# Performance work log

Hardware: AMD Instinct MI355X
Metric: run time of the kernel (lower is better)

The kernel has to match this reference:

```python
import jax, jax.numpy as jnp
from jax import lax
import numpy as np

N = 60000   # total nodes
B = 8       # graphs in batch
GS = N // B # nodes per graph
F = 384     # input node features
E = 600000  # edges
H = 6       # hiddenSize (hardcoded in source)
C = 10      # num_classes


def setup_inputs() -> dict:
    key = jax.random.key(0)
    ks = jax.random.split(key, 8)
    x = jax.random.normal(ks[0], (N, F), jnp.float32)
    src = jax.random.randint(ks[1], (E,), 0, N, jnp.int32)
    off = jax.random.randint(ks[2], (E,), 1, GS, jnp.int32)  # 1..GS-1 -> no self loops
    dst = (src // GS) * GS + (src % GS + off) % GS           # same-graph endpoint
    batch = jnp.arange(N, dtype=jnp.int32) // GS
    W1 = jax.random.normal(ks[3], (F, H), jnp.float32) * (1.0 / np.sqrt(F))
    b1 = jnp.zeros((H,), jnp.float32)
    W2 = jax.random.normal(ks[4], (H, C), jnp.float32) * (1.0 / np.sqrt(H))
    b2 = jnp.zeros((C,), jnp.float32)
    Wp1 = jax.random.normal(ks[5], (2 * H,), jnp.float32) * (1.0 / np.sqrt(2 * H))
    bp1 = jnp.zeros((), jnp.float32)
    Wp2 = jax.random.normal(ks[6], (2 * C,), jnp.float32) * (1.0 / np.sqrt(2 * C))
    bp2 = jnp.zeros((), jnp.float32)
    return dict(x=x, src=src, dst=dst, batch=batch, W1=W1, b1=b1, W2=W2, b2=b2,
                Wp1=Wp1, bp1=bp1, Wp2=Wp2, bp2=bp2)


def gcn_conv(x, src, dst, evalid, nvalid, W, b):
    # PyG GCNConv: h = x W; add remaining self-loops (weight 1); deg over dst;
    # norm = dinv[src]*dinv[dst]; aggregate to dst; + bias.
    n = x.shape[0]
    h = x @ W
    ef = evalid.astype(h.dtype)
    is_loop = evalid & (src == dst)
    has_loop = jax.ops.segment_sum(is_loop.astype(jnp.int32), dst, num_segments=n) > 0
    add_loop = (nvalid & ~has_loop).astype(h.dtype)
    deg = jax.ops.segment_sum(ef, dst, num_segments=n) + add_loop
    dinv = jnp.where(deg > 0, lax.rsqrt(jnp.maximum(deg, 1e-12)), 0.0)
    coef = ef * dinv[src] * dinv[dst]
    out = jax.ops.segment_sum(h[src] * coef[:, None], dst, num_segments=n)
    out = out + (add_loop * dinv * dinv)[:, None] * h
    return out + b


def edge_pool(x, src, dst, evalid, nvalid, Wp, bp):
    # PyG EdgePooling: raw = lin([x_src||x_dst]); score = softmax(raw, dst) + 0.5;
    # greedy contraction of edges by descending score; new_x = (sum over cluster) * score.
    n, f = x.shape
    raw = x[src] @ Wp[:f] + x[dst] @ Wp[f:] + bp                      # [E]
    rm = jnp.where(evalid, raw, -jnp.inf)
    m = jax.ops.segment_max(rm, dst, num_segments=n)
    m = jnp.where(jnp.isfinite(m), m, 0.0)
    ex = jnp.where(evalid, jnp.exp(raw - m[dst]), 0.0)
    s = jax.ops.segment_sum(ex, dst, num_segments=n)
    score = jnp.where(evalid, ex / jnp.where(s[dst] > 0, s[dst], 1.0), 0.0) + 0.5

    order = jnp.argsort(jnp.where(evalid, -score, jnp.inf))           # descending, invalid last

    def step(rem, edg):
        s_, d_, v_ = edg
        take = v_ & rem[s_] & rem[d_]
        rem = rem.at[s_].set(rem[s_] & ~take)
        rem = rem.at[d_].set(rem[d_] & ~take)
        return rem, take

    _, chosen_sorted = lax.scan(step, nvalid, (src[order], dst[order], evalid[order]))
    chosen = jnp.zeros_like(evalid).at[order].set(chosen_sorted)

    chf = chosen.astype(x.dtype)
    nonself = src != dst
    dead = jax.ops.segment_sum((chosen & nonself).astype(jnp.int32), dst, num_segments=n) > 0
    new_valid = nvalid & ~dead

    # merged feature: (x_src + x_dst) * score at slot src; unmatched: x * 1
    added = jnp.zeros_like(x).at[src].add((chf * nonself.astype(x.dtype))[:, None] * x[dst])
    scale = 1.0 + jnp.zeros((n,), x.dtype).at[src].add(chf * (score - 1.0))
    new_x = jnp.where(new_valid[:, None], (x + added) * scale[:, None], 0.0)

    # cluster map (dst of chosen edge -> src slot), remap + coalesce (dedup) edges
    merged_src = jnp.full((n,), -1, jnp.int32).at[dst].max(jnp.where(chosen, src, -1))
    cmap = jnp.where(merged_src >= 0, merged_src, jnp.arange(n, dtype=jnp.int32))
    ns, nd = cmap[src], cmap[dst]
    ns_k = jnp.where(evalid, ns, n)  # push invalid edges to the end
    order2 = jnp.lexsort((nd, ns_k))
    ss, dd = ns_k[order2], nd[order2]
    diff = (ss[1:] != ss[:-1]) | (dd[1:] != dd[:-1])
    first = jnp.concatenate([jnp.ones((1,), bool), diff])
    new_evalid = jnp.zeros_like(evalid).at[order2].set(first & evalid[order2])
    return new_x, ns, nd, new_evalid, new_valid


def _forward(x, src, dst, batch, W1, b1, W2, b2, Wp1, bp1, Wp2, bp2):
    evalid = jnp.ones((src.shape[0],), bool)
    nvalid = jnp.ones((x.shape[0],), bool)
    h = jax.nn.relu(gcn_conv(x, src, dst, evalid, nvalid, W1, b1))
    # dropout: identity in eval mode
    h, s1, d1, ev1, nv1 = edge_pool(h, src, dst, evalid, nvalid, Wp1, bp1)
    h = gcn_conv(h, s1, d1, ev1, nv1, W2, b2)
    h, s2, d2, ev2, nv2 = edge_pool(h, s1, d1, ev1, nv1, Wp2, bp2)
    nvf = nv2.astype(h.dtype)
    cnt = jax.ops.segment_sum(nvf, batch, num_segments=B)
    sm = jax.ops.segment_sum(h * nvf[:, None], batch, num_segments=B)
    g = sm / cnt[:, None]
    return jax.nn.log_softmax(g, axis=1)


def reference(x, src, dst, batch, W1, b1, W2, b2, Wp1, bp1, Wp2, bp2):
    return _forward(x, src, dst, batch, W1, b1, W2, b2, Wp1, bp1, Wp2, bp2)
```

## Files before the change

### kernel.cpp

```cpp
#include <hip/hip_runtime.h>
#include <math.h>

#define NN 60000
#define BB 8
#define GS 7500
#define FF 384
#define EE 600000
#define HH 6
#define CC 10
#define HT_BITS 20
#define HT_SIZE (1u << HT_BITS)
#define HT_MASK (HT_SIZE - 1u)
#define TPB 256
#define CAP 80000
#define REMW ((GS + 31) / 32)
#define GPAD 32
#define SCAN_B 1024
#define NBLK ((NN + SCAN_B - 1) / SCAN_B)
static_assert(NBLK <= 64, "scan2 assumes <=64 blocks");

static inline int ngrid(int n) { return (n + TPB - 1) / TPB; }

__device__ __forceinline__ unsigned long long mkprio(float sc, int e) {
  return (((unsigned long long)__float_as_uint(sc)) << 32) |
         (unsigned int)(~(unsigned int)e);
}

__global__ void k_mm1(const float* __restrict__ x, const float* __restrict__ W,
                      float* __restrict__ out) {
  __shared__ float Ws[FF * HH];
  for (int i = threadIdx.x; i < FF * HH; i += blockDim.x) Ws[i] = W[i];
  __syncthreads();
  int wave = threadIdx.x >> 6, lane = threadIdx.x & 63;
  int node = blockIdx.x * 4 + wave;
  if (node >= NN) return;
  const float* xr = x + (size_t)node * FF;
  float acc[HH] = {0.f, 0.f, 0.f, 0.f, 0.f, 0.f};
  for (int k = lane; k < FF; k += 64) {
    float xv = xr[k];
#pragma unroll
    for (int j = 0; j < HH; j++) acc[j] += xv * Ws[k * HH + j];
  }
#pragma unroll
  for (int j = 0; j < HH; j++) {
#pragma unroll
    for (int o = 32; o > 0; o >>= 1) acc[j] += __shfl_down(acc[j], o, 64);
  }
  if (lane == 0) {
#pragma unroll
    for (int j = 0; j < HH; j++) out[(size_t)node * HH + j] = acc[j];
  }
}

__global__ void k_prep(float* __restrict__ deg, unsigned char* __restrict__ hasloop,
                       int* __restrict__ gcntsA,
                       int* __restrict__ gcntsB, float* __restrict__ gsum,
                       float* __restrict__ gcnt, const unsigned char* __restrict__ nvin,
                       unsigned char* __restrict__ nvout, float* __restrict__ scale,
                       int* __restrict__ merged, int* __restrict__ partner,
                       unsigned long long* __restrict__ bestA,
                       unsigned long long* __restrict__ bestB,
                       unsigned char* __restrict__ remG) {
  int v = blockIdx.x * blockDim.x + threadIdx.x;
  if (v >= NN) return;
  deg[v] = 0.f;
  hasloop[v] = 0;
  unsigned char nvv = nvin ? nvin[v] : 1;
  nvout[v] = nvv;
  remG[v] = nvv;
  bestA[v] = 0ULL;
  bestB[v] = 0ULL;
  scale[v] = 1.0f;
  if (merged) merged[v] = -1;
  partner[v] = -1;
  if (v < BB * GPAD) { gcntsA[v] = 0; gcntsB[v] = 0; }
  if (v < BB * CC) gsum[v] = 0.f;
  if (v < BB) gcnt[v] = 0.f;
}

__global__ void k_deg(const int* __restrict__ src, const int* __restrict__ dst,
                      const unsigned char* __restrict__ ev, float* __restrict__ deg,
                      unsigned char* __restrict__ hasloop) {
  int e = blockIdx.x * blockDim.x + threadIdx.x;
  if (e >= EE) return;
  if (ev && !ev[e]) return;
  int d = dst[e];
  atomicAdd(&deg[d], 1.0f);
  if (src[e] == d) hasloop[d] = 1;
}

__global__ __launch_bounds__(1024) void k_scan1(const float* __restrict__ deg,
                                                int* __restrict__ rowstart,
                                                int* __restrict__ bsum) {
  __shared__ int tmp[SCAN_B];
  int t = threadIdx.x;
  int i = blockIdx.x * SCAN_B + t;
  int v = (i < NN) ? (int)deg[i] : 0;
  tmp[t] = v;
  __syncthreads();
  for (int o = 1; o < SCAN_B; o <<= 1) {
    int y = (t >= o) ? tmp[t - o] : 0;
    __syncthreads();
    tmp[t] += y;
    __syncthreads();
  }
  if (i < NN) rowstart[i] = tmp[t] - v;
  if (t == SCAN_B - 1) bsum[blockIdx.x] = tmp[t];
}

__global__ void k_scan2(int* __restrict__ bsum, int* __restrict__ rowstartNN) {
  int t = threadIdx.x;
  int v = (t < NBLK) ? bsum[t] : 0;
  int x = v;
#pragma unroll
  for (int o = 1; o < 64; o <<= 1) {
    int y = __shfl_up(x, o, 64);
    if (t >= o) x += y;
  }
  if (t < NBLK) bsum[t] = x - v;
  if (t == NBLK - 1) *rowstartNN = x;
}

__global__ void k_scan3(int* __restrict__ rowstart, const int* __restrict__ bsum,
                        int* __restrict__ fill, const float* __restrict__ deg,
                        const unsigned char* __restrict__ hasloop,
                        const unsigned char* __restrict__ nv, float* __restrict__ dinv,
                        unsigned char* __restrict__ addloop) {
  int i = blockIdx.x * blockDim.x + threadIdx.x;
  if (i >= NN) return;
  int r = rowstart[i] + bsum[i >> 10];
  rowstart[i] = r;
  fill[i] = r;
  int nvv = nv ? (int)nv[i] : 1;
  unsigned char al = (nvv && !hasloop[i]) ? 1 : 0;
  float d = deg[i] + (float)al;
  dinv[i] = d > 0.f ? 1.0f / sqrtf(fmaxf(d, 1e-12f)) : 0.f;
  addloop[i] = al;
}

__global__ void k_scatter(const int* __restrict__ src, const int* __restrict__ dst,
                          const unsigned char* __restrict__ ev, int* __restrict__ fill,
                          int* __restrict__ csrS, int* __restrict__ csrE) {
  int e = blockIdx.x * blockDim.x + threadIdx.x;
  if (e >= EE) return;
  if (ev && !ev[e]) return;
  int d = dst[e];
  int p = atomicAdd(&fill[d], 1);
  csrS[p] = src[e];
  csrE[p] = e;
}

template <int FD>
__global__ void k_agg_gather(const int* __restrict__ rowstart, const int* __restrict__ csrS,
                             const float* __restrict__ dinv, const float* __restrict__ h,
                             float* __restrict__ out) {
  int v = blockIdx.x * blockDim.x + threadIdx.x;
  if (v >= NN) return;
  int b0 = rowstart[v], b1 = rowstart[v + 1];
  float acc[FD];
#pragma unroll
  for (int j = 0; j < FD; j++) acc[j] = 0.f;
  float dv = dinv[v];
  for (int i = b0; i < b1; i++) {
    int s = csrS[i];
    float c = dinv[s] * dv;
    const float* hr = h + (size_t)s * FD;
#pragma unroll
    for (int j = 0; j < FD; j++) acc[j] += hr[j] * c;
  }
#pragma unroll
  for (int j = 0; j < FD; j++) out[(size_t)v * FD + j] = acc[j];
}

__global__ void k_gcn_fin(const float* __restrict__ h, const float* __restrict__ dinv,
                          const unsigned char* __restrict__ addloop, const float* __restrict__ b,
                          float* __restrict__ out, int fd, int relu) {
  int v = blockIdx.x * blockDim.x + threadIdx.x;
  if (v >= NN) return;
  float c = addloop[v] ? dinv[v] * dinv[v] : 0.f;
  for (int j = 0; j < fd; j++) {
    float o = out[(size_t)v * fd + j] + c * h[(size_t)v * fd + j] + b[j];
    if (relu) o = fmaxf(o, 0.f);
    out[(size_t)v * fd + j] = o;
  }
}

__global__ void k_raw(const float* __restrict__ x, const int* __restrict__ src,
                      const int* __restrict__ dst, const unsigned char* __restrict__ ev,
                      const float* __restrict__ Wp, const float* __restrict__ bp,
                      float* __restrict__ raw, int fd) {
  int e = blockIdx.x * blockDim.x + threadIdx.x;
  if (e >= EE) return;
  if (ev && !ev[e]) return;
  int s = src[e], d = dst[e];
  float r = bp[0];
  for (int j = 0; j < fd; j++) r += x[(size_t)s * fd + j] * Wp[j];
  for (int j = 0; j < fd; j++) r += x[(size_t)d * fd + j] * Wp[fd + j];
  raw[e] = r;
}

__global__ void k_sm_gather(const int* __restrict__ rowstart, const int* __restrict__ csrE,
                            const float* __restrict__ raw, float* __restrict__ mval,
                            float* __restrict__ ssum) {
  int v = blockIdx.x * blockDim.x + threadIdx.x;
  if (v >= NN) return;
  int b0 = rowstart[v], b1 = rowstart[v + 1];
  float m = -INFINITY;
  for (int i = b0; i < b1; i++) m = fmaxf(m, raw[csrE[i]]);
  if (b1 == b0) m = 0.f;
  float s = 0.f;
  for (int i = b0; i < b1; i++) s += expf(raw[csrE[i]] - m);
  mval[v] = m;
  ssum[v] = s;
}

__global__ void k_r1post(const int* __restrict__ src, const int* __restrict__ dst,
                         const float* __restrict__ raw, const float* __restrict__ mval,
                         const float* __restrict__ ssum,
                         const unsigned char* __restrict__ ev, const unsigned char* __restrict__ remG,
                         float* __restrict__ score, unsigned long long* __restrict__ bestA,
                         unsigned char* __restrict__ chosen) {
  int e = blockIdx.x * blockDim.x + threadIdx.x;
  if (e >= EE) return;
  chosen[e] = 0;
  if (ev && !ev[e]) return;
  int s = src[e], d = dst[e];
  if (!remG[s] || !remG[d]) return;
  float sd = ssum[d];
  float sc = expf(raw[e] - mval[d]) / (sd > 0.f ? sd : 1.0f) + 0.5f;
  score[e] = sc;
  unsigned long long p = mkprio(sc, e);
  if (p > bestA[s]) atomicMax(&bestA[s], p);
  if (d != s && p > bestA[d]) atomicMax(&bestA[d], p);
}

__global__ void k_r1sel(const int* __restrict__ src, const int* __restrict__ dst,
                        const float* __restrict__ score, const unsigned char* __restrict__ ev,
                        unsigned char* __restrict__ remG,
                        const unsigned long long* __restrict__ bestA,
                        unsigned long long* __restrict__ bestB,
                        unsigned char* __restrict__ chosen, ulonglong2* __restrict__ recs,
                        int* __restrict__ gcnts) {
  __shared__ int wcnt[TPB / 64][BB];
  __shared__ int bbase[BB];
  int e = blockIdx.x * blockDim.x + threadIdx.x;
  int w = threadIdx.x >> 6, lane = threadIdx.x & 63;
  int keep = 0, s = 0, d = 0, g = 0;
  unsigned long long p = 0;
  if (e < EE && (!ev || ev[e])) {
    s = src[e];
    d = dst[e];
    g = s / GS;
    if (remG[s] && remG[d]) {
      p = mkprio(score[e], e);
      if (bestA[s] == p && bestA[d] == p) {
        chosen[e] = 1;
        remG[s] = 0;
        remG[d] = 0;
      } else {
        keep = 1;
        bestB[s] = 0ULL;
        bestB[d] = 0ULL;
      }
    }
  }
  int myrank = 0;
#pragma unroll
  for (int gg = 0; gg < BB; gg++) {
    unsigned long long m = __ballot(keep && g == gg);
    if (keep && g == gg) myrank = __popcll(m & ((1ULL << lane) - 1ULL));
    if (lane == 0) wcnt[w][gg] = __popcll(m);
  }
  __syncthreads();
  if (threadIdx.x < BB) {
    int gg = threadIdx.x, tot = 0;
#pragma unroll
    for (int ww = 0; ww < TPB / 64; ww++) {
      int c = wcnt[ww][gg];
      wcnt[ww][gg] = tot;
      tot += c;
    }
    bbase[gg] = tot ? atomicAdd(&gcnts[gg * GPAD], tot) : 0;
  }
  __syncthreads();
  if (keep)
    recs[(size_t)g * CAP + bbase[g] + wcnt[w][g] + myrank] =
        make_ulonglong2(p, (((unsigned long long)(unsigned int)s) << 32) | (unsigned int)d);
}

__global__ void k_gpost(const ulonglong2* __restrict__ recs, const int* __restrict__ gcnts,
                        const unsigned char* __restrict__ remG,
                        unsigned long long* __restrict__ bestC, int* __restrict__ gcntsOut) {
  int g = blockIdx.y;
  if (blockIdx.x == 0 && threadIdx.x == 0) gcntsOut[g * GPAD] = 0;
  int n = gcnts[g * GPAD];
  const ulonglong2* lst = recs + (size_t)g * CAP;
  int stride = gridDim.x * blockDim.x;
  for (int i = blockIdx.x * blockDim.x + threadIdx.x; i < n; i += stride) {
    ulonglong2 r = lst[i];
    int s = (int)(r.y >> 32), d = (int)(r.y & 0xFFFFFFFFu);
    if (remG[s] && remG[d]) {
      if (r.x > bestC[s]) atomicMax(&bestC[s], r.x);
      if (d != s && r.x > bestC[d]) atomicMax(&bestC[d], r.x);
    }
  }
}

__global__ void k_gsel(const ulonglong2* __restrict__ recsIn, const int* __restrict__ gcntsIn,
                       unsigned char* __restrict__ remG,
                       const unsigned long long* __restrict__ bestC,
                       unsigned long long* __restrict__ bestN,
                       unsigned char* __restrict__ chosen, ulonglong2* __restrict__ recsOut,
                       int* __restrict__ gcntsOut) {
  int g = blockIdx.y;
  int n = gcntsIn[g * GPAD];
  const ulonglong2* lst = recsIn + (size_t)g * CAP;
  ulonglong2* outl = recsOut + (size_t)g * CAP;
  int lane = threadIdx.x & 63;
  int stride = gridDim.x * blockDim.x;
  for (int i = blockIdx.x * blockDim.x + threadIdx.x; i - lane < n; i += stride) {
    int keep = 0;
    ulonglong2 r;
    if (i < n) {
      r = lst[i];
      int s = (int)(r.y >> 32), d = (int)(r.y & 0xFFFFFFFFu);
      if (remG[s] && remG[d]) {
        if (bestC[s] == r.x && bestC[d] == r.x) {
          int e = (int)(~(unsigned int)(r.x & 0xFFFFFFFFu));
          chosen[e] = 1;
          remG[s] = 0;
          remG[d] = 0;
        } else {
          keep = 1;
          bestN[s] = 0ULL;
          bestN[d] = 0ULL;
        }
      }
    }
    unsigned long long m = __ballot(keep);
    int tot = __popcll(m);
    int pre = __popcll(m & ((1ULL << lane) - 1ULL));
    int b0 = 0;
    if (lane == 0 && tot) b0 = atomicAdd(&gcntsOut[g * GPAD], tot);
    b0 = __shfl(b0, 0, 64);
    if (keep) outl[b0 + pre] = r;
  }
}

__global__ __launch_bounds__(1024) void k_match_g(ulonglong2* __restrict__ recs0,
                                                  ulonglong2* __restrict__ recs1,
                                                  const int* __restrict__ gcnts,
                                                  const unsigned char* __restrict__ remG,
                                                  unsigned char* __restrict__ chosen) {
  __shared__ unsigned long long best[GS];
  __shared__ unsigned int remB[REMW];
  __shared__ int cnt_next;
  const int g = blockIdx.x;
  const int base = g * GS;
  const int t = threadIdx.x, nth = blockDim.x;
  const int lane = t & 63;

  for (int w = t; w < REMW; w += nth) {
    unsigned int bits = 0;
    int v0 = w * 32;
    if (v0 + 32 <= GS) {
      const unsigned int* p4 = (const unsigned int*)(remG + base + v0);
#pragma unroll
      for (int q = 0; q < 8; q++) {
        unsigned int x4 = p4[q];
        bits |= ((x4 & 1u) << (q * 4)) | (((x4 >> 8) & 1u) << (q * 4 + 1)) |
                (((x4 >> 16) & 1u) << (q * 4 + 2)) | (((x4 >> 24) & 1u) << (q * 4 + 3));
      }
    } else {
      for (int b = 0; b < 32; b++) {
        int v = v0 + b;
        if (v < GS) bits |= (remG[base + v] ? 1u : 0u) << b;
      }
    }
    remB[w] = bits;
  }
  for (int i = t; i < GS; i += nth) best[i] = 0ULL;
  __syncthreads();

  ulonglong2* bufs[2] = {recs0 + (size_t)g * CAP, recs1 + (size_t)g * CAP};
  int n = gcnts[g * GPAD];
  int cur = 0;
  int guard = 0;

  while (n > 0) {
    if (++guard > 100000) break;
    for (int i0 = 0; i0 < n; i0 += nth * 4) {
      ulonglong2 r[4];
      int have[4];
#pragma unroll
      for (int k = 0; k < 4; k++) {
        int i = i0 + t + k * nth;
        have[k] = i < n;
        if (have[k]) r[k] = bufs[cur][i];
      }
#pragma unroll
      for (int k = 0; k < 4; k++) {
        if (!have[k]) continue;
        int ls = (int)(r[k].y >> 32) - base, ld = (int)(r[k].y & 0xFFFFFFFFu) - base;
        if (((remB[ls >> 5] >> (ls & 31)) & 1u) && ((remB[ld >> 5] >> (ld & 31)) & 1u)) {
          if (r[k].x > best[ls]) atomicMax(&best[ls], r[k].x);
          if (ld != ls && r[k].x > best[ld]) atomicMax(&best[ld], r[k].x);
        }
      }
    }
    if (t == 0) cnt_next = 0;
    __syncthreads();
    for (int i0 = 0; i0 < n; i0 += nth * 4) {
      ulonglong2 r[4];
      int have[4];
#pragma unroll
      for (int k = 0; k < 4; k++) {
        int i = i0 + t + k * nth;
        have[k] = i < n;
        if (have[k]) r[k] = bufs[cur][i];
      }
#pragma unroll
      for (int k = 0; k < 4; k++) {
        int keep = 0;
        int ls = 0, ld = 0;
        if (have[k]) {
          ls = (int)(r[k].y >> 32) - base;
          ld = (int)(r[k].y & 0xFFFFFFFFu) - base;
          if (((remB[ls >> 5] >> (ls & 31)) & 1u) && ((remB[ld >> 5] >> (ld & 31)) & 1u)) {
            if (best[ls] == r[k].x && best[ld] == r[k].x) {
              int e = (int)(~(unsigned int)(r[k].x & 0xFFFFFFFFu));
              chosen[e] = 1;
              atomicAnd(&remB[ls >> 5], ~(1u << (ls & 31)));
              atomicAnd(&remB[ld >> 5], ~(1u << (ld & 31)));
            } else {
              keep = 1;
            }
          }
        }
        unsigned long long m = __ballot(keep);
        int tot = __popcll(m);
        int pre = __popcll(m & ((1ULL << lane) - 1ULL));
        int b0 = 0;
        if (lane == 0 && tot) b0 = atomicAdd(&cnt_next, tot);
        b0 = __shfl(b0, 0, 64);
        if (keep) bufs[cur ^ 1][b0 + pre] = r[k];
      }
    }
    __syncthreads();
    n = cnt_next;
    if (n < 4096) {
      for (int i = t; i < n; i += nth) {
        ulonglong2 r = bufs[cur ^ 1][i];
        best[(int)(r.y >> 32) - base] = 0ULL;
        best[(int)(r.y & 0xFFFFFFFFu) - base] = 0ULL;
      }
    } else {
      for (int i = t; i < GS; i += nth) best[i] = 0ULL;
    }
    __syncthreads();
    cur ^= 1;
  }
}

__global__ void k_pool_edge(const int* __restrict__ src, const int* __restrict__ dst,
                            const unsigned char* __restrict__ chosen, const float* __restrict__ score,
                            unsigned char* __restrict__ nvout, float* __restrict__ scale,
                            int* __restrict__ partner, int* __restrict__ merged) {
  int e = blockIdx.x * blockDim.x + threadIdx.x;
  if (e >= EE) return;
  if (!chosen[e]) return;
  int s = src[e], d = dst[e];
  scale[s] = score[e];
  if (merged) merged[d] = s;
  if (s != d) {
    nvout[d] = 0;
    partner[s] = d;
  }
}

__global__ void k_newx_mm2(const float* __restrict__ h1, const int* __restrict__ partner,
                           const float* __restrict__ scale, const unsigned char* __restrict__ nvout,
                           const float* __restrict__ W2, float* __restrict__ h2pre) {
  int v = blockIdx.x * blockDim.x + threadIdx.x;
  if (v >= NN) return;
  float sc = scale[v];
  int ok = nvout[v];
  int p = partner[v];
  float nx[HH];
#pragma unroll
  for (int j = 0; j < HH; j++) {
    float a = h1[(size_t)v * HH + j];
    if (p >= 0) a += h1[(size_t)p * HH + j];
    nx[j] = ok ? a * sc : 0.f;
  }
#pragma unroll
  for (int c = 0; c < CC; c++) {
    float a = 0.f;
#pragma unroll
    for (int j = 0; j < HH; j++) a += nx[j] * W2[j * CC + c];
    h2pre[(size_t)v * CC + c] = a;
  }
}

__device__ __forceinline__ unsigned int ht_hash(unsigned long long key) {
  return (unsigned int)((key * 0x9E3779B97F4A7C15ULL) >> 44) & HT_MASK;
}

__global__ void k_remap_ins(const int* __restrict__ src, const int* __restrict__ dst,
                            const int* __restrict__ merged, int* __restrict__ ns,
                            int* __restrict__ nd, unsigned long long* __restrict__ htab) {
  int e = blockIdx.x * blockDim.x + threadIdx.x;
  if (e >= EE) return;
  int s = src[e], d = dst[e];
  int ms = merged[s], md = merged[d];
  int a = ms >= 0 ? ms : s;
  int b = md >= 0 ? md : d;
  ns[e] = a;
  nd[e] = b;
  unsigned long long key =
      (unsigned long long)((((unsigned int)a) << 16) | (unsigned int)b);
  unsigned long long val = (key << 32) | (unsigned int)e;
  unsigned int h = ht_hash(key);
  for (;;) {
    unsigned long long curv = htab[h];
    if (curv == ~0ULL) {
      unsigned long long prev = atomicCAS(&htab[h], ~0ULL, val);
      if (prev == ~0ULL) break;
      curv = prev;
    }
    if ((curv >> 32) == key) {
      if ((curv & 0xFFFFFFFFULL) > (unsigned long long)(unsigned int)e)
        atomicMin(&htab[h], val);
      break;
    }
    h = (h + 1) & HT_MASK;
  }
}

__global__ void k_dedup_mark(const int* __restrict__ ns, const int* __restrict__ nd,
                             const unsigned long long* __restrict__ htab,
                             unsigned char* __restrict__ evout) {
  int e = blockIdx.x * blockDim.x + threadIdx.x;
  if (e >= EE) return;
  unsigned long long key =
      (unsigned long long)((((unsigned int)ns[e]) << 16) | (unsigned int)nd[e]);
  unsigned int h = ht_hash(key);
  for (;;) {
    unsigned long long curv = htab[h];
    if ((curv >> 32) == key) {
      evout[e] = ((curv & 0xFFFFFFFFULL) == (unsigned long long)(unsigned int)e) ? 1 : 0;
      return;
    }
    h = (h + 1) & HT_MASK;
  }
}

__global__ void k_newx_pool(const float* __restrict__ h2, const int* __restrict__ partner,
                            const float* __restrict__ scale, const unsigned char* __restrict__ nv,
                            float* __restrict__ gsum, float* __restrict__ gcnt) {
  int v = blockIdx.x * blockDim.x + threadIdx.x;
  int lane = threadIdx.x & 63;
  int b = (v < NN ? v : NN - 1) / GS;
  int active = (v < NN) && nv[v];
  float cnt = active ? 1.f : 0.f;
  float val[CC];
  if (active) {
    float sc = scale[v];
    int p = partner[v];
    for (int j = 0; j < CC; j++) {
      float a = h2[(size_t)v * CC + j];
      if (p >= 0) a += h2[(size_t)p * CC + j];
      val[j] = a * sc;
    }
  } else {
    for (int j = 0; j < CC; j++) val[j] = 0.f;
  }
  int b0 = __shfl(b, 0, 64);
  unsigned long long same = __ballot(b == b0);
  if (same == ~0ULL) {
    for (int o = 32; o > 0; o >>= 1) {
      cnt += __shfl_down(cnt, o, 64);
      for (int j = 0; j < CC; j++) val[j] += __shfl_down(val[j], o, 64);
    }
    if (lane == 0 && cnt > 0.f) {
      atomicAdd(&gcnt[b0], cnt);
      for (int j = 0; j < CC; j++) atomicAdd(&gsum[b0 * CC + j], val[j]);
    }
  } else if (active) {
    atomicAdd(&gcnt[b], cnt);
    for (int j = 0; j < CC; j++) atomicAdd(&gsum[b * CC + j], val[j]);
  }
}

__global__ void k_logsm(const float* __restrict__ gsum, const float* __restrict__ gcnt,
                        float* __restrict__ out) {
  int t = threadIdx.x;
  if (t >= BB) return;
  float gr[CC];
  float c = gcnt[t];
  float m = -INFINITY;
  for (int j = 0; j < CC; j++) {
    gr[j] = gsum[t * CC + j] / c;
    m = fmaxf(m, gr[j]);
  }
  float s = 0.f;
  for (int j = 0; j < CC; j++) s += expf(gr[j] - m);
  float l = logf(s);
  for (int j = 0; j < CC; j++) out[t * CC + j] = gr[j] - m - l;
}

extern "C" void kernel_launch(void* const* d_in, const int* in_sizes, int n_in,
                              void* d_out, int out_size, void* d_ws, size_t ws_size,
                              hipStream_t stream) {
  const float* x = (const float*)d_in[0];
  const int* src = (const int*)d_in[1];
  const int* dst = (const int*)d_in[2];
  const float* W1 = (const float*)d_in[4];
  const float* b1 = (const float*)d_in[5];
  const float* W2 = (const float*)d_in[6];
  const float* b2 = (const float*)d_in[7];
  const float* Wp1 = (const float*)d_in[8];
  const float* bp1 = (const float*)d_in[9];
  const float* Wp2 = (const float*)d_in[10];
  const float* bp2 = (const float*)d_in[11];
  float* out = (float*)d_out;

  char* wsb = (char*)d_ws;
  size_t off = 0;
  auto A = [&](size_t bytes) -> char* {
    char* r = wsb + off;
    off = (off + bytes + 255) & ~(size_t)255;
    return r;
  };
  float* h1pre = (float*)A((size_t)NN * HH * 4);
  float* h1out = (float*)A((size_t)NN * HH * 4);
  float* deg = (float*)A((size_t)NN * 4);
  float* dinv = (float*)A((size_t)NN * 4);
  unsigned char* hasloop = (unsigned char*)A(NN);
  unsigned char* addloop = (unsigned char*)A(NN);
  float* raw = (float*)A((size_t)EE * 4);
  float* score = (float*)A((size_t)EE * 4);
  float* mval = (float*)A((size_t)NN * 4);
  float* ssum = (float*)A((size_t)NN * 4);
  unsigned char* chosen = (unsigned char*)A(EE);
  unsigned char* nv1 = (unsigned char*)A(NN);
  unsigned char* nv2 = (unsigned char*)A(NN);
  float* scale = (float*)A((size_t)NN * 4);
  int* partner = (int*)A((size_t)NN * 4);
  int* merged = (int*)A((size_t)NN * 4);
  int* ns = (int*)A((size_t)EE * 4);
  int* nd = (int*)A((size_t)EE * 4);
  unsigned char* ev1 = (unsigned char*)A(EE);
  unsigned long long* htab = (unsigned long long*)A((size_t)HT_SIZE * 8);
  float* h2pre = (float*)A((size_t)NN * CC * 4);
  float* h2out = (float*)A((size_t)NN * CC * 4);
  unsigned long long* bestA = (unsigned long long*)A((size_t)NN * 8);
  unsigned long long* bestB = (unsigned long long*)A((size_t)NN * 8);
  unsigned char* remG = (unsigned char*)A(NN);
  ulonglong2* recs0 = (ulonglong2*)A((size_t)BB * CAP * 16);
  ulonglong2* recs1 = (ulonglong2*)A((size_t)BB * CAP * 16);
  int* gcntsA = (int*)A((size_t)BB * GPAD * 4);
  int* gcntsB = (int*)A((size_t)BB * GPAD * 4);
  float* gsum = (float*)A((size_t)BB * CC * 4);
  float* gcnt = (float*)A((size_t)BB * 4);
  int* rowstart = (int*)A((size_t)(NN + 1) * 4);
  int* fill = (int*)A((size_t)NN * 4);
  int* bsum = (int*)A((size_t)64 * 4);
  int* csrS = (int*)A((size_t)EE * 4);
  int* csrE = (int*)A((size_t)EE * 4);
  (void)ws_size; (void)n_in; (void)in_sizes; (void)out_size;

  const int GE = ngrid(EE), GN = ngrid(NN);
  const dim3 RG(32, BB);

  hipMemsetAsync(htab, 0xFF, (size_t)HT_SIZE * 8, stream);
  hipLaunchKernelGGL(k_mm1, dim3((NN + 3) / 4), dim3(TPB), 0, stream, x, W1, h1pre);
  hipLaunchKernelGGL(k_prep, dim3(GN), dim3(TPB), 0, stream, deg, hasloop, gcntsA, gcntsB,
                     gsum, gcnt, (const unsigned char*)nullptr, nv1, scale, merged, partner, bestA, bestB, remG);
  hipLaunchKernelGGL(k_deg, dim3(GE), dim3(TPB), 0, stream, src, dst, (const unsigned char*)nullptr, deg, hasloop);
  hipLaunchKernelGGL(k_scan1, dim3(NBLK), dim3(SCAN_B), 0, stream, deg, rowstart, bsum);
  hipLaunchKernelGGL(k_scan2, dim3(1), dim3(64), 0, stream, bsum, rowstart + NN);
  hipLaunchKernelGGL(k_scan3, dim3(GN), dim3(TPB), 0, stream, rowstart, bsum, fill, deg, hasloop,
                     (const unsigned char*)nullptr, dinv, addloop);
  hipLaunchKernelGGL(k_scatter, dim3(GE), dim3(TPB), 0, stream, src, dst, (const unsigned char*)nullptr, fill, csrS, csrE);
  hipLaunchKernelGGL(k_agg_gather<HH>, dim3(GN), dim3(TPB), 0, stream, rowstart, csrS, dinv, h1pre, h1out);
  hipLaunchKernelGGL(k_gcn_fin, dim3(GN), dim3(TPB), 0, stream, h1pre, dinv, addloop, b1, h1out, HH, 1);

  hipLaunchKernelGGL(k_raw, dim3(GE), dim3(TPB), 0, stream, h1out, src, dst, (const unsigned char*)nullptr, Wp1, bp1, raw, HH);
  hipLaunchKernelGGL(k_sm_gather, dim3(GN), dim3(TPB), 0, stream, rowstart, csrE, raw, mval, ssum);
  hipLaunchKernelGGL(k_r1post, dim3(GE), dim3(TPB), 0, stream, src, dst, raw, mval, ssum, (const unsigned char*)nullptr, remG, score, bestA, chosen);
  hipLaunchKernelGGL(k_r1sel, dim3(GE), dim3(TPB), 0, stream, src, dst, score, (const unsigned char*)nullptr, remG, bestA, bestB, chosen, recs0, gcntsA);
  hipLaunchKernelGGL(k_gpost, RG, dim3(TPB), 0, stream, recs0, gcntsA, remG, bestB, gcntsB);
  hipLaunchKernelGGL(k_gsel, RG, dim3(TPB), 0, stream, recs0, gcntsA, remG, bestB, bestA, chosen, recs1, gcntsB);
  hipLaunchKernelGGL(k_gpost, RG, dim3(TPB), 0, stream, recs1, gcntsB, remG, bestA, gcntsA);
  hipLaunchKernelGGL(k_gsel, RG, dim3(TPB), 0, stream, recs1, gcntsB, remG, bestA, bestB, chosen, recs0, gcntsA);
  hipLaunchKernelGGL(k_gpost, RG, dim3(TPB), 0, stream, recs0, gcntsA, remG, bestB, gcntsB);
  hipLaunchKernelGGL(k_gsel, RG, dim3(TPB), 0, stream, recs0, gcntsA, remG, bestB, bestA, chosen, recs1, gcntsB);
  hipLaunchKernelGGL(k_gpost, RG, dim3(TPB), 0, stream, recs1, gcntsB, remG, bestA, gcntsA);
  hipLaunchKernelGGL(k_gsel, RG, dim3(TPB), 0, stream, recs1, gcntsB, remG, bestA, bestB, chosen, recs0, gcntsA);
  hipLaunchKernelGGL(k_gpost, RG, dim3(TPB), 0, stream, recs0, gcntsA, remG, bestB, gcntsB);
  hipLaunchKernelGGL(k_gsel, RG, dim3(TPB), 0, stream, recs0, gcntsA, remG, bestB, bestA, chosen, recs1, gcntsB);
  hipLaunchKernelGGL(k_match_g, dim3(BB), dim3(1024), 0, stream, recs1, recs0, gcntsB, remG, chosen);
  hipLaunchKernelGGL(k_pool_edge, dim3(GE), dim3(TPB), 0, stream, src, dst, chosen, score, nv1, scale, partner, merged);
  hipLaunchKernelGGL(k_newx_mm2, dim3(GN), dim3(TPB), 0, stream, h1out, partner, scale, nv1, W2, h2pre);
  hipLaunchKernelGGL(k_remap_ins, dim3(GE), dim3(TPB), 0, stream, src, dst, merged, ns, nd, htab);
  hipLaunchKernelGGL(k_dedup_mark, dim3(GE), dim3(TPB), 0, stream, ns, nd, htab, ev1);

  hipLaunchKernelGGL(k_prep, dim3(GN), dim3(TPB), 0, stream, deg, hasloop, gcntsA, gcntsB,
                     gsum, gcnt, (const unsigned char*)nv1, nv2, scale, (int*)nullptr, partner, bestA, bestB, remG);
  hipLaunchKernelGGL(k_deg, dim3(GE), dim3(TPB), 0, stream, ns, nd, (const unsigned char*)ev1, deg, hasloop);
  hipLaunchKernelGGL(k_scan1, dim3(NBLK), dim3(SCAN_B), 0, stream, deg, rowstart, bsum);
  hipLaunchKernelGGL(k_scan2, dim3(1), dim3(64), 0, stream, bsum, rowstart + NN);
  hipLaunchKernelGGL(k_scan3, dim3(GN), dim3(TPB), 0, stream, rowstart, bsum, fill, deg, hasloop,
                     (const unsigned char*)nv1, dinv, addloop);
  hipLaunchKernelGGL(k_scatter, dim3(GE), dim3(TPB), 0, stream, ns, nd, (const unsigned char*)ev1, fill, csrS, csrE);
  hipLaunchKernelGGL(k_agg_gather<CC>, dim3(GN), dim3(TPB), 0, stream, rowstart, csrS, dinv, h2pre, h2out);
  hipLaunchKernelGGL(k_gcn_fin, dim3(GN), dim3(TPB), 0, stream, h2pre, dinv, addloop, b2, h2out, CC, 0);

  hipLaunchKernelGGL(k_raw, dim3(GE), dim3(TPB), 0, stream, h2out, ns, nd, (const unsigned char*)ev1, Wp2, bp2, raw, CC);
  hipLaunchKernelGGL(k_sm_gather, dim3(GN), dim3(TPB), 0, stream, rowstart, csrE, raw, mval, ssum);
  hipLaunchKernelGGL(k_r1post, dim3(GE), dim3(TPB), 0, stream, ns, nd, raw, mval, ssum, (const unsigned char*)ev1, remG, score, bestA, chosen);
  hipLaunchKernelGGL(k_r1sel, dim3(GE), dim3(TPB), 0, stream, ns, nd, score, (const unsigned char*)ev1, remG, bestA, bestB, chosen, recs0, gcntsA);
  hipLaunchKernelGGL(k_gpost, RG, dim3(TPB), 0, stream, recs0, gcntsA, remG, bestB, gcntsB);
  hipLaunchKernelGGL(k_gsel, RG, dim3(TPB), 0, stream, recs0, gcntsA, remG, bestB, bestA, chosen, recs1, gcntsB);
  hipLaunchKernelGGL(k_gpost, RG, dim3(TPB), 0, stream, recs1, gcntsB, remG, bestA, gcntsA);
  hipLaunchKernelGGL(k_gsel, RG, dim3(TPB), 0, stream, recs1, gcntsB, remG, bestA, bestB, chosen, recs0, gcntsA);
  hipLaunchKernelGGL(k_gpost, RG, dim3(TPB), 0, stream, recs0, gcntsA, remG, bestB, gcntsB);
  hipLaunchKernelGGL(k_gsel, RG, dim3(TPB), 0, stream, recs0, gcntsA, remG, bestB, bestA, chosen, recs1, gcntsB);
  hipLaunchKernelGGL(k_gpost, RG, dim3(TPB), 0, stream, recs1, gcntsB, remG, bestA, gcntsA);
  hipLaunchKernelGGL(k_gsel, RG, dim3(TPB), 0, stream, recs1, gcntsB, remG, bestA, bestB, chosen, recs0, gcntsA);
  hipLaunchKernelGGL(k_gpost, RG, dim3(TPB), 0, stream, recs0, gcntsA, remG, bestB, gcntsB);
  hipLaunchKernelGGL(k_gsel, RG, dim3(TPB), 0, stream, recs0, gcntsA, remG, bestB, bestA, chosen, recs1, gcntsB);
  hipLaunchKernelGGL(k_match_g, dim3(BB), dim3(1024), 0, stream, recs1, recs0, gcntsB, remG, chosen);
  hipLaunchKernelGGL(k_pool_edge, dim3(GE), dim3(TPB), 0, stream, ns, nd, chosen, score, nv2, scale, partner, (int*)nullptr);

  hipLaunchKernelGGL(k_newx_pool, dim3(GN), dim3(TPB), 0, stream, h2out, partner, scale, nv2, gsum, gcnt);
  hipLaunchKernelGGL(k_logsm, dim3(1), dim3(64), 0, stream, gsum, gcnt, out);
}
```

Before: 1.494 ms.

## Fuse GCN finalize into gather and softmax scoring into CSR pass

Merges the GCN aggregation and its self-loop/bias/ReLU finalize into one per-node kernel, so the intermediate output is not written and re-read. It also folds the per-destination softmax statistics and the per-edge score/priority kernel into a single CSR-walking kernel. That kernel keeps each node's best priority in a register and issues one atomic per node instead of one per edge. The chosen-flag reset moves to a memset, the mval/ssum buffers are dropped, and the pre-check before atomicMax in the matching loop is removed. The trade-off is a more serial per-node loop over a load-imbalanced CSR and possibly more atomics in the matching kernel.

```diff
diff --git a/kernel.cpp b/kernel.cpp
--- a/kernel.cpp
+++ b/kernel.cpp
@@ -151,9 +151,10 @@
 }
 
 template <int FD>
-__global__ void k_agg_gather(const int* __restrict__ rowstart, const int* __restrict__ csrS,
-                             const float* __restrict__ dinv, const float* __restrict__ h,
-                             float* __restrict__ out) {
+__global__ void k_agg_fin(const int* __restrict__ rowstart, const int* __restrict__ csrS,
+                          const float* __restrict__ dinv, const unsigned char* __restrict__ addloop,
+                          const float* __restrict__ h, const float* __restrict__ b,
+                          float* __restrict__ out, int relu) {
   int v = blockIdx.x * blockDim.x + threadIdx.x;
   if (v >= NN) return;
   int b0 = rowstart[v], b1 = rowstart[v + 1];
@@ -168,20 +169,13 @@
 #pragma unroll
     for (int j = 0; j < FD; j++) acc[j] += hr[j] * c;
   }
-#pragma unroll
-  for (int j = 0; j < FD; j++) out[(size_t)v * FD + j] = acc[j];
-}
-
-__global__ void k_gcn_fin(const float* __restrict__ h, const float* __restrict__ dinv,
-                          const unsigned char* __restrict__ addloop, const float* __restrict__ b,
-                          float* __restrict__ out, int fd, int relu) {
-  int v = blockIdx.x * blockDim.x + threadIdx.x;
-  if (v >= NN) return;
-  float c = addloop[v] ? dinv[v] * dinv[v] : 0.f;
-  for (int j = 0; j < fd; j++) {
-    float o = out[(size_t)v * fd + j] + c * h[(size_t)v * fd + j] + b[j];
+  float cl = addloop[v] ? dv * dv : 0.f;
+  const float* hv = h + (size_t)v * FD;
+#pragma unroll
+  for (int j = 0; j < FD; j++) {
+    float o = acc[j] + cl * hv[j] + b[j];
     if (relu) o = fmaxf(o, 0.f);
-    out[(size_t)v * fd + j] = o;
+    out[(size_t)v * FD + j] = o;
   }
 }
 
@@ -199,39 +193,32 @@
   raw[e] = r;
 }
 
-__global__ void k_sm_gather(const int* __restrict__ rowstart, const int* __restrict__ csrE,
-                            const float* __restrict__ raw, float* __restrict__ mval,
-                            float* __restrict__ ssum) {
+__global__ void k_smscore(const int* __restrict__ rowstart, const int* __restrict__ csrS,
+                          const int* __restrict__ csrE, const float* __restrict__ raw,
+                          const unsigned char* __restrict__ remG, float* __restrict__ score,
+                          unsigned long long* __restrict__ bestA) {
   int v = blockIdx.x * blockDim.x + threadIdx.x;
   if (v >= NN) return;
   int b0 = rowstart[v], b1 = rowstart[v + 1];
+  if (b0 == b1) return;
   float m = -INFINITY;
   for (int i = b0; i < b1; i++) m = fmaxf(m, raw[csrE[i]]);
-  if (b1 == b0) m = 0.f;
   float s = 0.f;
   for (int i = b0; i < b1; i++) s += expf(raw[csrE[i]] - m);
-  mval[v] = m;
-  ssum[v] = s;
-}
-
-__global__ void k_r1post(const int* __restrict__ src, const int* __restrict__ dst,
-                         const float* __restrict__ raw, const float* __restrict__ mval,
-                         const float* __restrict__ ssum,
-                         const unsigned char* __restrict__ ev, const unsigned char* __restrict__ remG,
-                         float* __restrict__ score, unsigned long long* __restrict__ bestA,
-                         unsigned char* __restrict__ chosen) {
-  int e = blockIdx.x * blockDim.x + threadIdx.x;
-  if (e >= EE) return;
-  chosen[e] = 0;
-  if (ev && !ev[e]) return;
-  int s = src[e], d = dst[e];
-  if (!remG[s] || !remG[d]) return;
-  float sd = ssum[d];
-  float sc = expf(raw[e] - mval[d]) / (sd > 0.f ? sd : 1.0f) + 0.5f;
-  score[e] = sc;
-  unsigned long long p = mkprio(sc, e);
-  if (p > bestA[s]) atomicMax(&bestA[s], p);
-  if (d != s && p > bestA[d]) atomicMax(&bestA[d], p);
+  if (!remG[v]) return;
+  float sd = s > 0.f ? s : 1.0f;
+  unsigned long long lb = 0ULL;
+  for (int i = b0; i < b1; i++) {
+    int sv = csrS[i];
+    if (!remG[sv]) continue;
+    int e = csrE[i];
+    float sc = expf(raw[e] - m) / sd + 0.5f;
+    score[e] = sc;
+    unsigned long long p = mkprio(sc, e);
+    if (p > lb) lb = p;
+    if (sv != v && p > bestA[sv]) atomicMax(&bestA[sv], p);
+  }
+  if (lb > bestA[v]) atomicMax(&bestA[v], lb);
 }
 
 __global__ void k_r1sel(const int* __restrict__ src, const int* __restrict__ dst,
@@ -403,8 +390,8 @@
         if (!have[k]) continue;
         int ls = (int)(r[k].y >> 32) - base, ld = (int)(r[k].y & 0xFFFFFFFFu) - base;
         if (((remB[ls >> 5] >> (ls & 31)) & 1u) && ((remB[ld >> 5] >> (ld & 31)) & 1u)) {
-          if (r[k].x > best[ls]) atomicMax(&best[ls], r[k].x);
-          if (ld != ls && r[k].x > best[ld]) atomicMax(&best[ld], r[k].x);
+          atomicMax(&best[ls], r[k].x);
+          if (ld != ls) atomicMax(&best[ld], r[k].x);
         }
       }
     }
@@ -640,8 +627,6 @@
   unsigned char* addloop = (unsigned char*)A(NN);
   float* raw = (float*)A((size_t)EE * 4);
   float* score = (float*)A((size_t)EE * 4);
-  float* mval = (float*)A((size_t)NN * 4);
-  float* ssum = (float*)A((size_t)NN * 4);
   unsigned char* chosen = (unsigned char*)A(EE);
   unsigned char* nv1 = (unsigned char*)A(NN);
   unsigned char* nv2 = (unsigned char*)A(NN);
@@ -683,12 +668,11 @@
   hipLaunchKernelGGL(k_scan3, dim3(GN), dim3(TPB), 0, stream, rowstart, bsum, fill, deg, hasloop,
                      (const unsigned char*)nullptr, dinv, addloop);
   hipLaunchKernelGGL(k_scatter, dim3(GE), dim3(TPB), 0, stream, src, dst, (const unsigned char*)nullptr, fill, csrS, csrE);
-  hipLaunchKernelGGL(k_agg_gather<HH>, dim3(GN), dim3(TPB), 0, stream, rowstart, csrS, dinv, h1pre, h1out);
-  hipLaunchKernelGGL(k_gcn_fin, dim3(GN), dim3(TPB), 0, stream, h1pre, dinv, addloop, b1, h1out, HH, 1);
+  hipLaunchKernelGGL(k_agg_fin<HH>, dim3(GN), dim3(TPB), 0, stream, rowstart, csrS, dinv, addloop, h1pre, b1, h1out, 1);
 
   hipLaunchKernelGGL(k_raw, dim3(GE), dim3(TPB), 0, stream, h1out, src, dst, (const unsigned char*)nullptr, Wp1, bp1, raw, HH);
-  hipLaunchKernelGGL(k_sm_gather, dim3(GN), dim3(TPB), 0, stream, rowstart, csrE, raw, mval, ssum);
-  hipLaunchKernelGGL(k_r1post, dim3(GE), dim3(TPB), 0, stream, src, dst, raw, mval, ssum, (const unsigned char*)nullptr, remG, score, bestA, chosen);
+  hipMemsetAsync(chosen, 0, (size_t)EE, stream);
+  hipLaunchKernelGGL(k_smscore, dim3(GN), dim3(TPB), 0, stream, rowstart, csrS, csrE, raw, remG, score, bestA);
   hipLaunchKernelGGL(k_r1sel, dim3(GE), dim3(TPB), 0, stream, src, dst, score, (const unsigned char*)nullptr, remG, bestA, bestB, chosen, recs0, gcntsA);
   hipLaunchKernelGGL(k_gpost, RG, dim3(TPB), 0, stream, recs0, gcntsA, remG, bestB, gcntsB);
   hipLaunchKernelGGL(k_gsel, RG, dim3(TPB), 0, stream, recs0, gcntsA, remG, bestB, bestA, chosen, recs1, gcntsB);
@@ -714,12 +698,11 @@
   hipLaunchKernelGGL(k_scan3, dim3(GN), dim3(TPB), 0, stream, rowstart, bsum, fill, deg, hasloop,
                      (const unsigned char*)nv1, dinv, addloop);
   hipLaunchKernelGGL(k_scatter, dim3(GE), dim3(TPB), 0, stream, ns, nd, (const unsigned char*)ev1, fill, csrS, csrE);
-  hipLaunchKernelGGL(k_agg_gather<CC>, dim3(GN), dim3(TPB), 0, stream, rowstart, csrS, dinv, h2pre, h2out);
-  hipLaunchKernelGGL(k_gcn_fin, dim3(GN), dim3(TPB), 0, stream, h2pre, dinv, addloop, b2, h2out, CC, 0);
+  hipLaunchKernelGGL(k_agg_fin<CC>, dim3(GN), dim3(TPB), 0, stream, rowstart, csrS, dinv, addloop, h2pre, b2, h2out, 0);
 
   hipLaunchKernelGGL(k_raw, dim3(GE), dim3(TPB), 0, stream, h2out, ns, nd, (const unsigned char*)ev1, Wp2, bp2, raw, CC);
-  hipLaunchKernelGGL(k_sm_gather, dim3(GN), dim3(TPB), 0, stream, rowstart, csrE, raw, mval, ssum);
-  hipLaunchKernelGGL(k_r1post, dim3(GE), dim3(TPB), 0, stream, ns, nd, raw, mval, ssum, (const unsigned char*)ev1, remG, score, bestA, chosen);
+  hipMemsetAsync(chosen, 0, (size_t)EE, stream);
+  hipLaunchKernelGGL(k_smscore, dim3(GN), dim3(TPB), 0, stream, rowstart, csrS, csrE, raw, remG, score, bestA);
   hipLaunchKernelGGL(k_r1sel, dim3(GE), dim3(TPB), 0, stream, ns, nd, score, (const unsigned char*)ev1, remG, bestA, bestB, chosen, recs0, gcntsA);
   hipLaunchKernelGGL(k_gpost, RG, dim3(TPB), 0, stream, recs0, gcntsA, remG, bestB, gcntsB);
   hipLaunchKernelGGL(k_gsel, RG, dim3(TPB), 0, stream, recs0, gcntsA, remG, bestB, bestA, chosen, recs1, gcntsB);
```

After: 1.469 ms. About the same (-1.6%).
